# Performance work log

Hardware: AMD Instinct MI355X
Metric: run time of the kernel (lower is better)

## Reference

```python
import jax, jax.numpy as jnp
import numpy as np

N_NODES = 15
EMBED_DIM = 2048
F1 = 1024
F2 = 512
N_EDGES = 120


def gcn_conv(x, src, dst, W, b):
    # PyG GCNConv: h = D^{-1/2} (A + I) D^{-1/2} (x W) + b
    h = x @ W                                   # [N, F_out]
    n = h.shape[0]
    loops = jnp.arange(n)
    s = jnp.concatenate([src, loops])
    d = jnp.concatenate([dst, loops])
    deg = jax.ops.segment_sum(jnp.ones_like(d, dtype=h.dtype), d, num_segments=n)
    dinv = jax.lax.rsqrt(deg)                   # deg >= 1 due to self loops
    norm = dinv[s] * dinv[d]                    # [E+N]
    out = jax.ops.segment_sum(h[s] * norm[:, None], d, num_segments=n)
    return out + b


def attention_pool(x, attW):
    # SimGNN-style attention: global ctx = tanh(mean(x W)); scores = sigmoid(x @ ctx)
    ctx = jnp.tanh(jnp.mean(x @ attW, axis=0))  # [F2]
    scores = jax.nn.sigmoid(x @ ctx)            # [N]
    return x.T @ scores                         # [F2]


def setup_inputs() -> dict:
    key = jax.random.key(0)
    ks = jax.random.split(key, 16)
    d = {}
    d['features_1'] = jax.random.normal(ks[0], (N_NODES,), dtype=jnp.float32)
    d['edge_index_1'] = jax.random.randint(ks[1], (2, N_EDGES), 0, N_NODES, dtype=jnp.int32)
    d['target'] = jax.random.uniform(ks[2], (3,), dtype=jnp.float32)
    def lin(k, fi, fo):
        s = 1.0 / np.sqrt(fi)
        kw, kb = jax.random.split(k)
        return (jax.random.uniform(kw, (fi, fo), minval=-s, maxval=s, dtype=jnp.float32),
                jax.random.uniform(kb, (fo,), minval=-s, maxval=s, dtype=jnp.float32))
    d['W1'], d['b1'] = lin(ks[3], 15, 15 * 32)
    d['W2'], d['b2'] = lin(ks[4], 15 * 32, 15 * 128)
    d['W3'], d['b3'] = lin(ks[5], 15 * 128, 15 * EMBED_DIM)
    d['gW1'], d['gb1'] = lin(ks[6], EMBED_DIM, F1)
    d['gW2'], d['gb2'] = lin(ks[7], F1, F2)
    d['attW'] = jax.random.normal(ks[8], (F2, F2), dtype=jnp.float32) * (1.0 / np.sqrt(F2))
    d['fcW'], d['fcb'] = lin(ks[9], F2, 3)
    return d


def reference(features_1, edge_index_1, target, W1, b1, W2, b2, W3, b3,
              gW1, gb1, gW2, gb2, attW, fcW, fcb):
    # embed MLP: 15 -> 480 -> 1920 -> 15*embed_dim
    h = jax.nn.relu(features_1 @ W1 + b1)
    h = jax.nn.relu(h @ W2 + b2)
    h = (h @ W3 + b3).reshape(N_NODES, EMBED_DIM)
    src, dst = edge_index_1[0], edge_index_1[1]
    x = jax.nn.relu(gcn_conv(h, src, dst, gW1, gb1))
    x = gcn_conv(x, src, dst, gW2, gb2)
    rep = attention_pool(x, attW)               # [F2]
    logits = rep @ fcW + fcb                    # [3]
    cls = jnp.argmax(target)
    loss = -jax.nn.log_softmax(logits)[cls]
    predictions = jax.nn.softmax(logits)
    return loss, predictions
```

## Files before the change

### kernel.cpp

```cpp
#include <hip/hip_runtime.h>
#include <math.h>

#define NN 15
#define EMBED 2048
#define F1D 1024
#define F2D 512
#define NE 120
#define H1_DIM 480
#define H2_DIM 1920
#define H3_DIM 30720

#define OFF_H2   0
#define OFF_H3   2048
#define OFF_T1   32768
#define OFF_T2   48128
#define OFF_X1   55808
#define OFF_X2   71168
#define OFF_A    78848
#define OFF_CTX  79104

__device__ inline void f4ma(float4& a, float s, const float4& w) {
    a.x += s * w.x; a.y += s * w.y; a.z += s * w.z; a.w += s * w.w;
}
__device__ inline void f4acc(float4& a, const float4& b) {
    a.x += b.x; a.y += b.y; a.z += b.z; a.w += b.w;
}

__global__ void k0_setup(const int* __restrict__ edges, float* __restrict__ ws) {
    __shared__ float dinv[NN];
    __shared__ float A[NN * NN];
    int tid = threadIdx.x;
    if (tid < NN) {
        int deg = 1;
        for (int i = 0; i < NE; ++i) deg += (edges[NE + i] == tid) ? 1 : 0;
        dinv[tid] = rsqrtf((float)deg);
    }
    __syncthreads();
    if (tid < NN * NN) {
        int r = tid / NN, c = tid % NN;
        A[tid] = (r == c) ? dinv[r] * dinv[r] : 0.0f;
    }
    __syncthreads();
    if (tid == 0) {
        for (int i = 0; i < NE; ++i) {
            int s = edges[i], d = edges[NE + i];
            A[d * NN + s] += dinv[s] * dinv[d];
        }
    }
    __syncthreads();
    if (tid < NN * NN) ws[OFF_A + tid] = A[tid];
    for (int i = tid; i < 23040; i += 256) ws[OFF_T1 + i] = 0.0f;
}

__global__ void k1_h2(const float* __restrict__ f, const float* __restrict__ W1,
                      const float* __restrict__ b1, const float* __restrict__ W2,
                      const float* __restrict__ b2, float* __restrict__ ws) {
    __shared__ float h1[H1_DIM];
    __shared__ float4 red[32][8];
    int tid = threadIdx.x;
    float fr[NN];
#pragma unroll
    for (int k = 0; k < NN; ++k) fr[k] = f[k];
    for (int j = tid; j < H1_DIM; j += 256) {
        float acc = b1[j];
#pragma unroll
        for (int k = 0; k < NN; ++k) acc += fr[k] * W1[k * H1_DIM + j];
        h1[j] = fmaxf(acc, 0.0f);
    }
    __syncthreads();
    int jg = tid & 7, kc = tid >> 3;
    int j = blockIdx.x * 32 + jg * 4;
    float4 acc = make_float4(0.f, 0.f, 0.f, 0.f);
    for (int r = 0; r < 15; ++r) {
        int k = kc * 15 + r;
        float4 w = *(const float4*)(W2 + k * H2_DIM + j);
        f4ma(acc, h1[k], w);
    }
    red[kc][jg] = acc;
    __syncthreads();
    for (int s = 16; s >= 1; s >>= 1) {
        if (kc < s) f4acc(red[kc][jg], red[kc + s][jg]);
        __syncthreads();
    }
    if (kc == 0) {
        float4 b = *(const float4*)(b2 + j);
        float4 v = red[0][jg];
        v.x = fmaxf(v.x + b.x, 0.f); v.y = fmaxf(v.y + b.y, 0.f);
        v.z = fmaxf(v.z + b.z, 0.f); v.w = fmaxf(v.w + b.w, 0.f);
        *(float4*)(ws + OFF_H2 + j) = v;
    }
}

__global__ void k2_h3(const float* __restrict__ W3, const float* __restrict__ b3,
                      float* __restrict__ ws) {
    __shared__ float h2[H2_DIM];
    __shared__ float4 red[16][16];
    int tid = threadIdx.x;
    {
        const float4* g = (const float4*)(ws + OFF_H2);
        float4* l = (float4*)h2;
        for (int i = tid; i < H2_DIM / 4; i += 256) l[i] = g[i];
    }
    __syncthreads();
    int jg = tid & 15, kc = tid >> 4;
    int j = blockIdx.x * 64 + jg * 4;
    float4 acc = make_float4(0.f, 0.f, 0.f, 0.f);
    const float* wp = W3 + (size_t)(kc * 120) * H3_DIM + j;
    const float* hp = h2 + kc * 120;
#pragma unroll 8
    for (int r = 0; r < 120; ++r) {
        float4 w = *(const float4*)wp;
        f4ma(acc, hp[r], w);
        wp += H3_DIM;
    }
    red[kc][jg] = acc;
    __syncthreads();
    for (int s = 8; s >= 1; s >>= 1) {
        if (kc < s) f4acc(red[kc][jg], red[kc + s][jg]);
        __syncthreads();
    }
    if (kc == 0) {
        float4 b = *(const float4*)(b3 + j);
        float4 v = red[0][jg];
        v.x += b.x; v.y += b.y; v.z += b.z; v.w += b.w;
        *(float4*)(ws + OFF_H3 + j) = v;
    }
}

template<int IN, int OUT, int ECH>
__global__ void k_mm15(const float* __restrict__ X, const float* __restrict__ W,
                       float* __restrict__ Acc) {
    __shared__ float4 red[16][16][15];
    float* hbuf = (float*)red;
    int tid = threadIdx.x;
    int e0 = blockIdx.y * ECH;
    int f0 = blockIdx.x * 64;
    for (int i = tid; i < NN * ECH; i += 256) {
        int n = i / ECH, e = i - n * ECH;
        hbuf[i] = X[n * IN + e0 + e];
    }
    __syncthreads();
    int fg = tid & 15, kt = tid >> 4;
    int f = f0 + fg * 4;
    float4 acc[NN];
#pragma unroll
    for (int n = 0; n < NN; ++n) acc[n] = make_float4(0.f, 0.f, 0.f, 0.f);
    const int RPT = ECH / 16;
    for (int r = 0; r < RPT; ++r) {
        int e = kt * RPT + r;
        float4 w = *(const float4*)(W + (size_t)(e0 + e) * OUT + f);
#pragma unroll
        for (int n = 0; n < NN; ++n) f4ma(acc[n], hbuf[n * ECH + e], w);
    }
    __syncthreads();
#pragma unroll
    for (int n = 0; n < NN; ++n) red[kt][fg][n] = acc[n];
    __syncthreads();
    for (int s = 8; s >= 1; s >>= 1) {
        if (kt < s) {
#pragma unroll
            for (int n = 0; n < NN; ++n) f4acc(red[kt][fg][n], red[kt + s][fg][n]);
        }
        __syncthreads();
    }
    if (kt == 0) {
#pragma unroll
        for (int n = 0; n < NN; ++n) {
            float4 v = red[0][fg][n];
            atomicAdd(&Acc[n * OUT + f + 0], v.x);
            atomicAdd(&Acc[n * OUT + f + 1], v.y);
            atomicAdd(&Acc[n * OUT + f + 2], v.z);
            atomicAdd(&Acc[n * OUT + f + 3], v.w);
        }
    }
}

template<int F, bool RELU>
__global__ void k_agg(const float* __restrict__ T, const float* __restrict__ bias,
                      const float* __restrict__ Amat, float* __restrict__ Xout) {
    int n = blockIdx.x;
    int f = threadIdx.x * 4;
    float4 acc = *(const float4*)(bias + f);
#pragma unroll
    for (int m = 0; m < NN; ++m) {
        float a = Amat[n * NN + m];
        float4 t = *(const float4*)(T + m * F + f);
        f4ma(acc, a, t);
    }
    if (RELU) {
        acc.x = fmaxf(acc.x, 0.f); acc.y = fmaxf(acc.y, 0.f);
        acc.z = fmaxf(acc.z, 0.f); acc.w = fmaxf(acc.w, 0.f);
    }
    *(float4*)(Xout + n * F + f) = acc;
}

__global__ void k7_ctx(const float* __restrict__ attW, float* __restrict__ ws) {
    __shared__ float xbar[F2D];
    __shared__ float4 red[64][4];
    int tid = threadIdx.x;
    const float* x2 = ws + OFF_X2;
    for (int e = tid; e < F2D; e += 256) {
        float s = 0.f;
#pragma unroll
        for (int n = 0; n < NN; ++n) s += x2[n * F2D + e];
        xbar[e] = s * (1.0f / 15.0f);
    }
    __syncthreads();
    int fg = tid & 3, kt = tid >> 2;
    int f = blockIdx.x * 16 + fg * 4;
    float4 acc = make_float4(0.f, 0.f, 0.f, 0.f);
    for (int r = 0; r < 8; ++r) {
        int e = kt * 8 + r;
        float4 w = *(const float4*)(attW + e * F2D + f);
        f4ma(acc, xbar[e], w);
    }
    red[kt][fg] = acc;
    __syncthreads();
    for (int s = 32; s >= 1; s >>= 1) {
        if (kt < s) f4acc(red[kt][fg], red[kt + s][fg]);
        __syncthreads();
    }
    if (kt == 0) {
        float4 v = red[0][fg];
        ws[OFF_CTX + f + 0] = tanhf(v.x);
        ws[OFF_CTX + f + 1] = tanhf(v.y);
        ws[OFF_CTX + f + 2] = tanhf(v.z);
        ws[OFF_CTX + f + 3] = tanhf(v.w);
    }
}

__global__ void k8_final(const float* __restrict__ fcW, const float* __restrict__ fcb,
                         const float* __restrict__ target, const float* __restrict__ ws,
                         float* __restrict__ out) {
    __shared__ float x2l[NN * F2D];
    __shared__ float ctxl[F2D];
    __shared__ float scores[16];
    __shared__ float rep[F2D];
    __shared__ float logits[3];
    int tid = threadIdx.x;
    const float* x2 = ws + OFF_X2;
    for (int i = tid; i < NN * F2D; i += 256) x2l[i] = x2[i];
    for (int i = tid; i < F2D; i += 256) ctxl[i] = ws[OFF_CTX + i];
    __syncthreads();
    {
        int g = tid >> 4, l = tid & 15;
        if (g < NN) {
            float p = 0.f;
            for (int i = 0; i < 32; ++i) {
                int e = l + 16 * i;
                p += x2l[g * F2D + e] * ctxl[e];
            }
            p += __shfl_xor(p, 1); p += __shfl_xor(p, 2);
            p += __shfl_xor(p, 4); p += __shfl_xor(p, 8);
            if (l == 0) scores[g] = 1.0f / (1.0f + expf(-p));
        }
    }
    __syncthreads();
    for (int fi = tid; fi < F2D; fi += 256) {
        float v = 0.f;
#pragma unroll
        for (int n = 0; n < NN; ++n) v += x2l[n * F2D + fi] * scores[n];
        rep[fi] = v;
    }
    __syncthreads();
    if (tid < 192) {
        int j = tid >> 6, l = tid & 63;
        float p = 0.f;
        for (int i = 0; i < 8; ++i) {
            int e = l + 64 * i;
            p += rep[e] * fcW[e * 3 + j];
        }
        p += __shfl_xor(p, 1); p += __shfl_xor(p, 2); p += __shfl_xor(p, 4);
        p += __shfl_xor(p, 8); p += __shfl_xor(p, 16); p += __shfl_xor(p, 32);
        if (l == 0) logits[j] = p + fcb[j];
    }
    __syncthreads();
    if (tid == 0) {
        float t0 = target[0], t1 = target[1], t2 = target[2];
        int cls = 0; float best = t0;
        if (t1 > best) { best = t1; cls = 1; }
        if (t2 > best) { cls = 2; }
        float l0 = logits[0], l1 = logits[1], l2 = logits[2];
        float m = fmaxf(l0, fmaxf(l1, l2));
        float e0 = expf(l0 - m), e1 = expf(l1 - m), e2 = expf(l2 - m);
        float s = e0 + e1 + e2;
        float lc = (cls == 0) ? l0 : ((cls == 1) ? l1 : l2);
        out[0] = -(lc - m - logf(s));
        out[1] = e0 / s; out[2] = e1 / s; out[3] = e2 / s;
    }
}

extern "C" void kernel_launch(void* const* d_in, const int* in_sizes, int n_in,
                              void* d_out, int out_size, void* d_ws, size_t ws_size,
                              hipStream_t stream) {
    const float* f    = (const float*)d_in[0];
    const int*   ei   = (const int*)d_in[1];
    const float* tgt  = (const float*)d_in[2];
    const float* W1   = (const float*)d_in[3];
    const float* b1   = (const float*)d_in[4];
    const float* W2   = (const float*)d_in[5];
    const float* b2   = (const float*)d_in[6];
    const float* W3   = (const float*)d_in[7];
    const float* b3   = (const float*)d_in[8];
    const float* gW1  = (const float*)d_in[9];
    const float* gb1  = (const float*)d_in[10];
    const float* gW2  = (const float*)d_in[11];
    const float* gb2  = (const float*)d_in[12];
    const float* attW = (const float*)d_in[13];
    const float* fcW  = (const float*)d_in[14];
    const float* fcb  = (const float*)d_in[15];
    float* ws  = (float*)d_ws;
    float* out = (float*)d_out;

    k0_setup<<<dim3(1), dim3(256), 0, stream>>>(ei, ws);
    k1_h2<<<dim3(60), dim3(256), 0, stream>>>(f, W1, b1, W2, b2, ws);
    k2_h3<<<dim3(480), dim3(256), 0, stream>>>(W3, b3, ws);
    k_mm15<2048, 1024, 128><<<dim3(16, 16), dim3(256), 0, stream>>>(ws + OFF_H3, gW1, ws + OFF_T1);
    k_agg<1024, true><<<dim3(15), dim3(256), 0, stream>>>(ws + OFF_T1, gb1, ws + OFF_A, ws + OFF_X1);
    k_mm15<1024, 512, 64><<<dim3(8, 16), dim3(256), 0, stream>>>(ws + OFF_X1, gW2, ws + OFF_T2);
    k_agg<512, false><<<dim3(15), dim3(128), 0, stream>>>(ws + OFF_T2, gb2, ws + OFF_A, ws + OFF_X2);
    k7_ctx<<<dim3(32), dim3(256), 0, stream>>>(attW, ws);
    k8_final<<<dim3(1), dim3(256), 0, stream>>>(fcW, fcb, tgt, ws, out);
}
```

Baseline: 413.7 us.

## Reassociate GCN aggregation before weight matmul and replace atomics with split-K partials

The pipeline is restructured so the normalized adjacency is applied before each GCN weight matmul, which is valid because A(XW) = (AX)W. Atomic accumulation is replaced by per-K-chunk partial buffers that separate reduce kernels sum. The adjacency setup is folded into the first kernel as an extra block, and the W3 GEMV is re-tiled into a 2D split-K grid with wider column tiles. This removes the separate setup and zeroing kernel and the atomic contention, at the cost of more workspace traffic for the partials and extra reduction kernels.

After: 411.0 us. No clear change (-0.7%).

```diff
diff --git a/kernel.cpp b/kernel.cpp
--- a/kernel.cpp
+++ b/kernel.cpp
@@ -10,14 +10,16 @@
 #define H2_DIM 1920
 #define H3_DIM 30720
 
-#define OFF_H2   0
-#define OFF_H3   2048
-#define OFF_T1   32768
-#define OFF_T2   48128
-#define OFF_X1   55808
-#define OFF_X2   71168
-#define OFF_A    78848
-#define OFF_CTX  79104
+#define OFF_A    0
+#define OFF_H2   256
+#define OFF_P3   2304
+#define OFF_XG1  248064
+#define OFF_P1   278784
+#define OFF_XG2  524544
+#define OFF_P2   539904
+#define OFF_X2   662784
+#define OFF_XBAR 670464
+#define OFF_CTX  670976
 
 __device__ inline void f4ma(float4& a, float s, const float4& w) {
     a.x += s * w.x; a.y += s * w.y; a.z += s * w.z; a.w += s * w.w;
@@ -26,38 +28,37 @@
     a.x += b.x; a.y += b.y; a.z += b.z; a.w += b.w;
 }
 
-__global__ void k0_setup(const int* __restrict__ edges, float* __restrict__ ws) {
-    __shared__ float dinv[NN];
-    __shared__ float A[NN * NN];
-    int tid = threadIdx.x;
-    if (tid < NN) {
-        int deg = 1;
-        for (int i = 0; i < NE; ++i) deg += (edges[NE + i] == tid) ? 1 : 0;
-        dinv[tid] = rsqrtf((float)deg);
-    }
-    __syncthreads();
-    if (tid < NN * NN) {
-        int r = tid / NN, c = tid % NN;
-        A[tid] = (r == c) ? dinv[r] * dinv[r] : 0.0f;
-    }
-    __syncthreads();
-    if (tid == 0) {
-        for (int i = 0; i < NE; ++i) {
-            int s = edges[i], d = edges[NE + i];
-            A[d * NN + s] += dinv[s] * dinv[d];
-        }
-    }
-    __syncthreads();
-    if (tid < NN * NN) ws[OFF_A + tid] = A[tid];
-    for (int i = tid; i < 23040; i += 256) ws[OFF_T1 + i] = 0.0f;
-}
-
 __global__ void k1_h2(const float* __restrict__ f, const float* __restrict__ W1,
                       const float* __restrict__ b1, const float* __restrict__ W2,
-                      const float* __restrict__ b2, float* __restrict__ ws) {
+                      const float* __restrict__ b2, const int* __restrict__ edges,
+                      float* __restrict__ ws) {
+    int tid = threadIdx.x;
+    if (blockIdx.x == 60) {
+        __shared__ float dinv[NN];
+        __shared__ float A[NN * NN];
+        if (tid < NN) {
+            int deg = 1;
+            for (int i = 0; i < NE; ++i) deg += (edges[NE + i] == tid) ? 1 : 0;
+            dinv[tid] = rsqrtf((float)deg);
+        }
+        __syncthreads();
+        if (tid < NN * NN) {
+            int r = tid / NN, c = tid % NN;
+            A[tid] = (r == c) ? dinv[r] * dinv[r] : 0.0f;
+        }
+        __syncthreads();
+        if (tid == 0) {
+            for (int i = 0; i < NE; ++i) {
+                int s = edges[i], d = edges[NE + i];
+                A[d * NN + s] += dinv[s] * dinv[d];
+            }
+        }
+        __syncthreads();
+        if (tid < NN * NN) ws[OFF_A + tid] = A[tid];
+        return;
+    }
     __shared__ float h1[H1_DIM];
     __shared__ float4 red[32][8];
-    int tid = threadIdx.x;
     float fr[NN];
 #pragma unroll
     for (int k = 0; k < NN; ++k) fr[k] = f[k];
@@ -91,72 +92,85 @@
     }
 }
 
-__global__ void k2_h3(const float* __restrict__ W3, const float* __restrict__ b3,
-                      float* __restrict__ ws) {
-    __shared__ float h2[H2_DIM];
-    __shared__ float4 red[16][16];
-    int tid = threadIdx.x;
-    {
-        const float4* g = (const float4*)(ws + OFF_H2);
-        float4* l = (float4*)h2;
-        for (int i = tid; i < H2_DIM / 4; i += 256) l[i] = g[i];
-    }
-    __syncthreads();
-    int jg = tid & 15, kc = tid >> 4;
-    int j = blockIdx.x * 64 + jg * 4;
+__global__ void k2_h3(const float* __restrict__ W3, float* __restrict__ ws) {
+    __shared__ float h2l[240];
+    __shared__ float4 red[128];
+    int tid = threadIdx.x;
+    int cb = blockIdx.x, kc = blockIdx.y;
+    int kbase = kc * 240;
+    for (int i = tid; i < 240; i += 256) h2l[i] = ws[OFF_H2 + kbase + i];
+    __syncthreads();
+    int f4i = tid & 127, rg = tid >> 7;
+    int col = cb * 512 + f4i * 4;
     float4 acc = make_float4(0.f, 0.f, 0.f, 0.f);
-    const float* wp = W3 + (size_t)(kc * 120) * H3_DIM + j;
-    const float* hp = h2 + kc * 120;
+    const float* wp = W3 + (size_t)(kbase + rg) * H3_DIM + col;
 #pragma unroll 8
-    for (int r = 0; r < 120; ++r) {
+    for (int i = 0; i < 120; ++i) {
         float4 w = *(const float4*)wp;
-        f4ma(acc, hp[r], w);
-        wp += H3_DIM;
-    }
-    red[kc][jg] = acc;
-    __syncthreads();
-    for (int s = 8; s >= 1; s >>= 1) {
-        if (kc < s) f4acc(red[kc][jg], red[kc + s][jg]);
-        __syncthreads();
-    }
-    if (kc == 0) {
-        float4 b = *(const float4*)(b3 + j);
-        float4 v = red[0][jg];
-        v.x += b.x; v.y += b.y; v.z += b.z; v.w += b.w;
-        *(float4*)(ws + OFF_H3 + j) = v;
+        f4ma(acc, h2l[2 * i + rg], w);
+        wp += 2 * (size_t)H3_DIM;
+    }
+    if (rg == 1) red[f4i] = acc;
+    __syncthreads();
+    if (rg == 0) {
+        f4acc(acc, red[f4i]);
+        *(float4*)(ws + OFF_P3 + (size_t)kc * H3_DIM + col) = acc;
+    }
+}
+
+__global__ void k3_agg1(const float* __restrict__ b3, float* __restrict__ ws) {
+    __shared__ float Al[NN * NN];
+    __shared__ float S[NN][32];
+    int tid = threadIdx.x;
+    int c0 = blockIdx.x * 32;
+    for (int i = tid; i < NN * NN; i += 256) Al[i] = ws[OFF_A + i];
+    for (int q = tid; q < NN * 32; q += 256) {
+        int m = q >> 5, c = q & 31;
+        int j = m * EMBED + c0 + c;
+        float s = b3[j];
+#pragma unroll
+        for (int p = 0; p < 8; ++p) s += ws[OFF_P3 + p * H3_DIM + j];
+        S[m][c] = s;
+    }
+    __syncthreads();
+    for (int q = tid; q < NN * 32; q += 256) {
+        int n = q >> 5, c = q & 31;
+        float x = 0.f;
+#pragma unroll
+        for (int m = 0; m < NN; ++m) x += Al[n * NN + m] * S[m][c];
+        ws[OFF_XG1 + n * EMBED + c0 + c] = x;
     }
 }
 
 template<int IN, int OUT, int ECH>
-__global__ void k_mm15(const float* __restrict__ X, const float* __restrict__ W,
-                       float* __restrict__ Acc) {
-    __shared__ float4 red[16][16][15];
-    float* hbuf = (float*)red;
+__global__ void k_mmP(const float* __restrict__ X, const float* __restrict__ W,
+                      float* __restrict__ P) {
+    __shared__ float Xl[NN * ECH];
+    __shared__ float4 red[8][32][NN];
     int tid = threadIdx.x;
     int e0 = blockIdx.y * ECH;
-    int f0 = blockIdx.x * 64;
     for (int i = tid; i < NN * ECH; i += 256) {
         int n = i / ECH, e = i - n * ECH;
-        hbuf[i] = X[n * IN + e0 + e];
-    }
-    __syncthreads();
-    int fg = tid & 15, kt = tid >> 4;
-    int f = f0 + fg * 4;
+        Xl[i] = X[n * IN + e0 + e];
+    }
+    __syncthreads();
+    int fg = tid & 31, kt = tid >> 5;
+    int f = blockIdx.x * 128 + fg * 4;
     float4 acc[NN];
 #pragma unroll
     for (int n = 0; n < NN; ++n) acc[n] = make_float4(0.f, 0.f, 0.f, 0.f);
-    const int RPT = ECH / 16;
+    const int RPT = ECH / 8;
     for (int r = 0; r < RPT; ++r) {
         int e = kt * RPT + r;
         float4 w = *(const float4*)(W + (size_t)(e0 + e) * OUT + f);
 #pragma unroll
-        for (int n = 0; n < NN; ++n) f4ma(acc[n], hbuf[n * ECH + e], w);
+        for (int n = 0; n < NN; ++n) f4ma(acc[n], Xl[n * ECH + e], w);
     }
     __syncthreads();
 #pragma unroll
     for (int n = 0; n < NN; ++n) red[kt][fg][n] = acc[n];
     __syncthreads();
-    for (int s = 8; s >= 1; s >>= 1) {
+    for (int s = 4; s >= 1; s >>= 1) {
         if (kt < s) {
 #pragma unroll
             for (int n = 0; n < NN; ++n) f4acc(red[kt][fg][n], red[kt + s][fg][n]);
@@ -167,44 +181,60 @@
 #pragma unroll
         for (int n = 0; n < NN; ++n) {
             float4 v = red[0][fg][n];
-            atomicAdd(&Acc[n * OUT + f + 0], v.x);
-            atomicAdd(&Acc[n * OUT + f + 1], v.y);
-            atomicAdd(&Acc[n * OUT + f + 2], v.z);
-            atomicAdd(&Acc[n * OUT + f + 3], v.w);
-        }
-    }
-}
-
-template<int F, bool RELU>
-__global__ void k_agg(const float* __restrict__ T, const float* __restrict__ bias,
-                      const float* __restrict__ Amat, float* __restrict__ Xout) {
-    int n = blockIdx.x;
-    int f = threadIdx.x * 4;
-    float4 acc = *(const float4*)(bias + f);
-#pragma unroll
-    for (int m = 0; m < NN; ++m) {
-        float a = Amat[n * NN + m];
-        float4 t = *(const float4*)(T + m * F + f);
-        f4ma(acc, a, t);
-    }
-    if (RELU) {
-        acc.x = fmaxf(acc.x, 0.f); acc.y = fmaxf(acc.y, 0.f);
-        acc.z = fmaxf(acc.z, 0.f); acc.w = fmaxf(acc.w, 0.f);
-    }
-    *(float4*)(Xout + n * F + f) = acc;
-}
-
-__global__ void k7_ctx(const float* __restrict__ attW, float* __restrict__ ws) {
-    __shared__ float xbar[F2D];
+            *(float4*)(P + (size_t)blockIdx.y * NN * OUT + n * OUT + f) = v;
+        }
+    }
+}
+
+__global__ void k5_fin1(const float* __restrict__ gb1, float* __restrict__ ws) {
+    __shared__ float Al[NN * NN];
+    __shared__ float S[NN][64];
+    int tid = threadIdx.x;
+    int f0 = blockIdx.x * 64;
+    for (int i = tid; i < NN * NN; i += 256) Al[i] = ws[OFF_A + i];
+    for (int q = tid; q < NN * 64; q += 256) {
+        int n = q >> 6, c = q & 63;
+        float s = gb1[f0 + c];
+#pragma unroll
+        for (int p = 0; p < 16; ++p) s += ws[OFF_P1 + p * (NN * F1D) + n * F1D + f0 + c];
+        S[n][c] = fmaxf(s, 0.f);
+    }
+    __syncthreads();
+    for (int q = tid; q < NN * 64; q += 256) {
+        int n = q >> 6, c = q & 63;
+        float x = 0.f;
+#pragma unroll
+        for (int m = 0; m < NN; ++m) x += Al[n * NN + m] * S[m][c];
+        ws[OFF_XG2 + n * F1D + f0 + c] = x;
+    }
+}
+
+__global__ void k7_fin2(const float* __restrict__ gb2, float* __restrict__ ws) {
+    __shared__ float S[NN][64];
+    int tid = threadIdx.x;
+    int f0 = blockIdx.x * 64;
+    for (int q = tid; q < NN * 64; q += 256) {
+        int n = q >> 6, c = q & 63;
+        float s = gb2[f0 + c];
+#pragma unroll
+        for (int p = 0; p < 16; ++p) s += ws[OFF_P2 + p * (NN * F2D) + n * F2D + f0 + c];
+        S[n][c] = s;
+        ws[OFF_X2 + n * F2D + f0 + c] = s;
+    }
+    __syncthreads();
+    if (tid < 64) {
+        float s = 0.f;
+#pragma unroll
+        for (int n = 0; n < NN; ++n) s += S[n][tid];
+        ws[OFF_XBAR + f0 + tid] = s * (1.0f / 15.0f);
+    }
+}
+
+__global__ void k8_ctx(const float* __restrict__ attW, float* __restrict__ ws) {
+    __shared__ float xb[F2D];
     __shared__ float4 red[64][4];
     int tid = threadIdx.x;
-    const float* x2 = ws + OFF_X2;
-    for (int e = tid; e < F2D; e += 256) {
-        float s = 0.f;
-#pragma unroll
-        for (int n = 0; n < NN; ++n) s += x2[n * F2D + e];
-        xbar[e] = s * (1.0f / 15.0f);
-    }
+    for (int e = tid; e < F2D; e += 256) xb[e] = ws[OFF_XBAR + e];
     __syncthreads();
     int fg = tid & 3, kt = tid >> 2;
     int f = blockIdx.x * 16 + fg * 4;
@@ -212,7 +242,7 @@
     for (int r = 0; r < 8; ++r) {
         int e = kt * 8 + r;
         float4 w = *(const float4*)(attW + e * F2D + f);
-        f4ma(acc, xbar[e], w);
+        f4ma(acc, xb[e], w);
     }
     red[kt][fg] = acc;
     __syncthreads();
@@ -229,7 +259,7 @@
     }
 }
 
-__global__ void k8_final(const float* __restrict__ fcW, const float* __restrict__ fcb,
+__global__ void k9_final(const float* __restrict__ fcW, const float* __restrict__ fcb,
                          const float* __restrict__ target, const float* __restrict__ ws,
                          float* __restrict__ out) {
     __shared__ float x2l[NN * F2D];
@@ -238,8 +268,7 @@
     __shared__ float rep[F2D];
     __shared__ float logits[3];
     int tid = threadIdx.x;
-    const float* x2 = ws + OFF_X2;
-    for (int i = tid; i < NN * F2D; i += 256) x2l[i] = x2[i];
+    for (int i = tid; i < NN * F2D; i += 256) x2l[i] = ws[OFF_X2 + i];
     for (int i = tid; i < F2D; i += 256) ctxl[i] = ws[OFF_CTX + i];
     __syncthreads();
     {
@@ -312,13 +341,13 @@
     float* ws  = (float*)d_ws;
     float* out = (float*)d_out;
 
-    k0_setup<<<dim3(1), dim3(256), 0, stream>>>(ei, ws);
-    k1_h2<<<dim3(60), dim3(256), 0, stream>>>(f, W1, b1, W2, b2, ws);
-    k2_h3<<<dim3(480), dim3(256), 0, stream>>>(W3, b3, ws);
-    k_mm15<2048, 1024, 128><<<dim3(16, 16), dim3(256), 0, stream>>>(ws + OFF_H3, gW1, ws + OFF_T1);
-    k_agg<1024, true><<<dim3(15), dim3(256), 0, stream>>>(ws + OFF_T1, gb1, ws + OFF_A, ws + OFF_X1);
-    k_mm15<1024, 512, 64><<<dim3(8, 16), dim3(256), 0, stream>>>(ws + OFF_X1, gW2, ws + OFF_T2);
-    k_agg<512, false><<<dim3(15), dim3(128), 0, stream>>>(ws + OFF_T2, gb2, ws + OFF_A, ws + OFF_X2);
-    k7_ctx<<<dim3(32), dim3(256), 0, stream>>>(attW, ws);
-    k8_final<<<dim3(1), dim3(256), 0, stream>>>(fcW, fcb, tgt, ws, out);
-}
+    k1_h2<<<dim3(61), dim3(256), 0, stream>>>(f, W1, b1, W2, b2, ei, ws);
+    k2_h3<<<dim3(60, 8), dim3(256), 0, stream>>>(W3, ws);
+    k3_agg1<<<dim3(64), dim3(256), 0, stream>>>(b3, ws);
+    k_mmP<2048, 1024, 128><<<dim3(8, 16), dim3(256), 0, stream>>>(ws + OFF_XG1, gW1, ws + OFF_P1);
+    k5_fin1<<<dim3(16), dim3(256), 0, stream>>>(gb1, ws);
+    k_mmP<1024, 512, 64><<<dim3(4, 16), dim3(256), 0, stream>>>(ws + OFF_XG2, gW2, ws + OFF_P2);
+    k7_fin2<<<dim3(8), dim3(256), 0, stream>>>(gb2, ws);
+    k8_ctx<<<dim3(32), dim3(256), 0, stream>>>(attW, ws);
+    k9_final<<<dim3(1), dim3(256), 0, stream>>>(fcW, fcb, tgt, ws, out);
+}
```
